# Performance work log

Measured on AMD Instinct MI355X. Metric: run time of the kernel, lower is better.

Reference implementation:

```python
import jax, jax.numpy as jnp
import numpy as np

HEADS = 16
D_MODEL = 1024
D_K = D_MODEL // HEADS
BATCH = 4
SEQ = 1024
NEG_BIG = -1000000000.0


def setup_inputs() -> dict:
    key = jax.random.key(0)
    ks = jax.random.split(key, 7)
    s = 1.0 / np.sqrt(D_MODEL)
    return {
        "q": jax.random.normal(ks[0], (BATCH, SEQ, D_MODEL), jnp.float32),
        "k": jax.random.normal(ks[1], (BATCH, SEQ, D_MODEL), jnp.float32),
        "v": jax.random.normal(ks[2], (BATCH, SEQ, D_MODEL), jnp.float32),
        "Wq": jax.random.normal(ks[3], (D_MODEL, D_MODEL), jnp.float32) * s,
        "Wk": jax.random.normal(ks[4], (D_MODEL, D_MODEL), jnp.float32) * s,
        "Wv": jax.random.normal(ks[5], (D_MODEL, D_MODEL), jnp.float32) * s,
        "Wo": jax.random.normal(ks[6], (D_MODEL, D_MODEL), jnp.float32) * s,
    }


def reference(q, k, v, Wq, Wk, Wv, Wo):
    bs = q.shape[0]
    residual = q
    # torch Linear(bias=False): x @ W.T ; then the module's quirky reshape
    # view(bs, h, -1, d_k) on the contiguous [bs, seq, d_model] buffer.
    qh = (q @ Wq.T).reshape(bs, HEADS, -1, D_K)   # [b, h, s, d_k]
    kh = (k @ Wk.T).reshape(bs, HEADS, -1, D_K)
    vh = (v @ Wv.T).reshape(bs, HEADS, -1, D_K)
    scores = jnp.einsum("bhqd,bhkd->bhqk", qh, kh) / jnp.sqrt(
        jnp.asarray(D_K, qh.dtype))
    # data-dependent mask: exact-zero scores get -1e9 before softmax
    scores = jnp.where(scores == 0, jnp.asarray(NEG_BIG, scores.dtype), scores)
    attn = jax.nn.softmax(scores, axis=-1)  # dropout is identity in eval mode
    out = jnp.einsum("bhqk,bhkd->bhqd", attn, vh)  # [b, h, s, d_k]
    concat = jnp.swapaxes(out, 1, 2).reshape(bs, -1, D_MODEL)
    return concat @ Wo.T + residual
```

## Files before the change

### kernel.cpp

```cpp
#include <hip/hip_runtime.h>
#include <stdint.h>

typedef __bf16 bf16x8 __attribute__((ext_vector_type(8)));
typedef __bf16 bf16x2v __attribute__((ext_vector_type(2)));
typedef float f32x4 __attribute__((ext_vector_type(4)));
typedef uint16_t u16x8 __attribute__((ext_vector_type(8)));
typedef uint32_t u32x2 __attribute__((ext_vector_type(2)));
typedef short s16x4 __attribute__((ext_vector_type(4)));

#define DMODEL 1024
#define K1SC 0.1803368801111244f

__device__ __forceinline__ uint16_t bfc(float f) {
  __bf16 h = (__bf16)f;
  return __builtin_bit_cast(uint16_t, h);
}
__device__ __forceinline__ uint32_t pk32(float a, float b) {
  bf16x2v t = {(__bf16)a, (__bf16)b};
  return __builtin_bit_cast(uint32_t, t);
}
__device__ __forceinline__ void gld16(const void* src, void* dst) {
  __builtin_amdgcn_global_load_lds((const __attribute__((address_space(1))) void*)src,
                                   (__attribute__((address_space(3))) void*)dst, 16, 0, 0);
}

__global__ __launch_bounds__(256, 2)
void gemm_qkv_kernel(const float* __restrict__ A0, const float* __restrict__ A1,
                     const float* __restrict__ A2, const float* __restrict__ W0,
                     const float* __restrict__ W1, const float* __restrict__ W2,
                     uint16_t* __restrict__ C0, uint16_t* __restrict__ C1,
                     uint16_t* __restrict__ C2) {
  int orig = blockIdx.x;
  int lin = (orig & 7) * 96 + (orig >> 3);
  int z = lin >> 8, rem = lin & 255;
  int m0 = (rem >> 3) * 128, n0 = (rem & 7) * 128;

  const float* A  = z == 0 ? A0 : (z == 1 ? A1 : A2);
  const float* Bw = z == 0 ? W0 : (z == 1 ? W1 : W2);
  uint16_t* C = z == 0 ? C0 : (z == 1 ? C1 : C2);
  const float osc = (z == 0) ? K1SC : 1.0f;

  __shared__ __align__(16) char As[2][128 * 64];
  __shared__ __align__(16) char Bs[2][128 * 64];
  const int t = threadIdx.x;
  const int lane = t & 63;
  const int w = t >> 6;
  const int wr = w >> 1, wc = w & 1;
  const int lr = lane & 15, ksl = lane >> 4;

  const int srow = t >> 2, sch = t & 3;
  const float* pa = A + (size_t)(m0 + srow) * DMODEL + sch * 8;
  const float* pb = Bw + (size_t)(n0 + srow) * DMODEL + sch * 8;
  const int sd = srow * 64 + ((sch ^ (srow & 3)) * 16);

  f32x4 la0, la1, la2, la3, lb0, lb1, lb2, lb3;
  auto LOAD = [&]() {
    la0 = *(const f32x4*)pa;           la1 = *(const f32x4*)(pa + 4);
    la2 = *(const f32x4*)(pa + 65536); la3 = *(const f32x4*)(pa + 65540);
    lb0 = *(const f32x4*)pb;           lb1 = *(const f32x4*)(pb + 4);
    lb2 = *(const f32x4*)(pb + 65536); lb3 = *(const f32x4*)(pb + 65540);
  };
  auto pack2 = [](f32x4 x, f32x4 y) {
    u16x8 r;
#pragma unroll
    for (int j = 0; j < 4; ++j) { r[j] = bfc(x[j]); r[4 + j] = bfc(y[j]); }
    return r;
  };
  auto STORE = [&](int buf) {
    char* ab = &As[buf][0];
    char* bb = &Bs[buf][0];
    *(u16x8*)(ab + sd) = pack2(la0, la1);
    *(u16x8*)(ab + sd + 4096) = pack2(la2, la3);
    *(u16x8*)(bb + sd) = pack2(lb0, lb1);
    *(u16x8*)(bb + sd + 4096) = pack2(lb2, lb3);
  };

  f32x4 acc[4][4];
#pragma unroll
  for (int m = 0; m < 4; ++m)
#pragma unroll
    for (int n = 0; n < 4; ++n) acc[m][n] = (f32x4){0.f, 0.f, 0.f, 0.f};

  LOAD();
  STORE(0);
  __syncthreads();

  const int co = (ksl ^ (lr & 3)) * 16;

  int cur = 0;
#pragma unroll 1
  for (int kt = 0; kt < 32; ++kt) {
    if (kt < 31) { pa += 32; pb += 32; LOAD(); }
    const char* Ab = &As[cur][0];
    const char* Bb = &Bs[cur][0];
    bf16x8 af[4], bfv[4];
#pragma unroll
    for (int m = 0; m < 4; ++m)
      af[m] = *(const bf16x8*)(Ab + (wr * 64 + m * 16 + lr) * 64 + co);
#pragma unroll
    for (int n = 0; n < 4; ++n)
      bfv[n] = *(const bf16x8*)(Bb + (wc * 64 + n * 16 + lr) * 64 + co);
    __builtin_amdgcn_s_setprio(1);
#pragma unroll
    for (int m = 0; m < 4; ++m)
#pragma unroll
      for (int n = 0; n < 4; ++n)
        acc[m][n] = __builtin_amdgcn_mfma_f32_16x16x32_bf16(af[m], bfv[n], acc[m][n], 0, 0, 0);
    __builtin_amdgcn_s_setprio(0);
    if (kt < 31) STORE(cur ^ 1);
    __syncthreads();
    cur ^= 1;
  }

#pragma unroll
  for (int m = 0; m < 4; ++m) {
#pragma unroll
    for (int n = 0; n < 4; ++n) {
      int col = n0 + wc * 64 + n * 16 + lr;
#pragma unroll
      for (int r = 0; r < 4; ++r) {
        int row = m0 + wr * 64 + m * 16 + ksl * 4 + r;
        C[(size_t)row * DMODEL + col] = bfc(acc[m][n][r] * osc);
      }
    }
  }
}

__global__ __launch_bounds__(256, 4)
void gemm_o_kernel(const uint16_t* __restrict__ Ac, const float* __restrict__ Bw,
                   float* __restrict__ Cf, const float* __restrict__ resid) {
  int orig = blockIdx.x;
  int lin = (orig & 7) * 64 + (orig >> 3);
  int m0 = (lin >> 3) * 64, n0 = (lin & 7) * 128;

  __shared__ __align__(16) char As[2][64 * 64];
  __shared__ __align__(16) char Bs[2][128 * 64];
  const int t = threadIdx.x;
  const int lane = t & 63;
  const int w = t >> 6;
  const int wr = w >> 1, wc = w & 1;
  const int lr = lane & 15, ksl = lane >> 4;

  const int srow = t >> 2, sch = t & 3;
  const uint16_t* pc = Ac + (size_t)(m0 + srow) * DMODEL + sch * 8;
  const float* pb = Bw + (size_t)(n0 + srow) * DMODEL + sch * 8;
  const int sd = srow * 64 + ((sch ^ (srow & 3)) * 16);

  u16x8 lc;
  f32x4 lb0, lb1, lb2, lb3;
  auto LOAD = [&]() {
    lc = *(const u16x8*)pc;
    lb0 = *(const f32x4*)pb;           lb1 = *(const f32x4*)(pb + 4);
    lb2 = *(const f32x4*)(pb + 65536); lb3 = *(const f32x4*)(pb + 65540);
  };
  auto pack2 = [](f32x4 x, f32x4 y) {
    u16x8 r;
#pragma unroll
    for (int j = 0; j < 4; ++j) { r[j] = bfc(x[j]); r[4 + j] = bfc(y[j]); }
    return r;
  };
  auto STORE = [&](int buf) {
    *(u16x8*)(&As[buf][0] + sd) = lc;
    char* bb = &Bs[buf][0];
    *(u16x8*)(bb + sd) = pack2(lb0, lb1);
    *(u16x8*)(bb + sd + 4096) = pack2(lb2, lb3);
  };

  f32x4 acc[2][4];
#pragma unroll
  for (int m = 0; m < 2; ++m)
#pragma unroll
    for (int n = 0; n < 4; ++n) acc[m][n] = (f32x4){0.f, 0.f, 0.f, 0.f};

  LOAD();
  STORE(0);
  __syncthreads();

  const int co = (ksl ^ (lr & 3)) * 16;

  int cur = 0;
#pragma unroll 1
  for (int kt = 0; kt < 32; ++kt) {
    if (kt < 31) { pc += 32; pb += 32; LOAD(); }
    const char* Ab = &As[cur][0];
    const char* Bb = &Bs[cur][0];
    bf16x8 af[2], bfv[4];
#pragma unroll
    for (int m = 0; m < 2; ++m)
      af[m] = *(const bf16x8*)(Ab + (wr * 32 + m * 16 + lr) * 64 + co);
#pragma unroll
    for (int n = 0; n < 4; ++n)
      bfv[n] = *(const bf16x8*)(Bb + (wc * 64 + n * 16 + lr) * 64 + co);
    __builtin_amdgcn_s_setprio(1);
#pragma unroll
    for (int m = 0; m < 2; ++m)
#pragma unroll
      for (int n = 0; n < 4; ++n)
        acc[m][n] = __builtin_amdgcn_mfma_f32_16x16x32_bf16(af[m], bfv[n], acc[m][n], 0, 0, 0);
    __builtin_amdgcn_s_setprio(0);
    if (kt < 31) STORE(cur ^ 1);
    __syncthreads();
    cur ^= 1;
  }

#pragma unroll
  for (int m = 0; m < 2; ++m) {
#pragma unroll
    for (int n = 0; n < 4; ++n) {
      int col = n0 + wc * 64 + n * 16 + lr;
#pragma unroll
      for (int r = 0; r < 4; ++r) {
        int row = m0 + wr * 32 + m * 16 + ksl * 4 + r;
        size_t idx = (size_t)row * DMODEL + col;
        Cf[idx] = acc[m][n][r] + resid[idx];
      }
    }
  }
}

__global__ __launch_bounds__(256, 4)
void attn_mfma_kernel(const uint16_t* __restrict__ Pq, const uint16_t* __restrict__ Pk,
                      const uint16_t* __restrict__ Pv, uint16_t* __restrict__ Cc) {
  __shared__ __align__(16) uint16_t Ks[2][64 * 64];
  __shared__ __align__(16) uint16_t Vts[2][64 * 64];

  const int t = threadIdx.x;
  const int w = t >> 6;
  const int lane = t & 63;
  const int lr = lane & 15;
  const int ksl = lane >> 4;
  int orig = blockIdx.x;
  int lin = (orig & 7) * 128 + (orig >> 3);
  const int bh = lin >> 4, qt = lin & 15;
  const int b = bh >> 4, h = bh & 15;

  const uint16_t* Qb = Pq + (size_t)bh * 65536 + (size_t)qt * 4096;
  const uint16_t* Kb = Pk + (size_t)bh * 65536;
  const uint16_t* Vb = Pv + (size_t)bh * 65536;

  bf16x8 qf0, qf1;
  {
    const uint16_t* qrow = Qb + (size_t)(w * 16 + lr) * 64 + ksl * 8;
    qf0 = *(const bf16x8*)(qrow);
    qf1 = *(const bf16x8*)(qrow + 32);
  }

  f32x4 Oa[4];
#pragma unroll
  for (int n = 0; n < 4; ++n) Oa[n] = (f32x4){0.f, 0.f, 0.f, 0.f};
  f32x4 lsum4 = {0.f, 0.f, 0.f, 0.f};

  const int sw = (lr & 7) << 4;
  const int p2 = t & 31;
  const int c8 = t >> 5;

  int qko[4][2], pvo[4][4], wvo[8];
#pragma unroll
  for (int n = 0; n < 4; ++n) {
#pragma unroll
    for (int c = 0; c < 2; ++c) qko[n][c] = (n * 16 + lr) * 128 + ((c * 64 + ksl * 16) ^ sw);
#pragma unroll
    for (int nd = 0; nd < 4; ++nd) pvo[n][nd] = (nd * 16 + lr) * 128 + ((n * 32 + ksl * 8) ^ sw);
  }
#pragma unroll
  for (int i = 0; i < 8; ++i) {
    int d = c8 * 8 + i;
    wvo[i] = d * 128 + ((p2 * 4) ^ ((d & 7) << 4));
  }

  const int sr0 = t >> 3;
  const int sc0 = (((t & 7) * 16) ^ ((sr0 & 7) << 4)) >> 1;
  const uint16_t* srcK = Kb + (size_t)sr0 * 64 + sc0;
  const uint16_t* srcV = Vb + (size_t)(p2 * 2) * 64 + c8 * 8;
  const int kd0 = t * 16, kd1 = (256 + t) * 16;

  char* kb0 = (char*)&Ks[0][0];
  char* kb1 = (char*)&Ks[1][0];
  char* vb0 = (char*)&Vts[0][0];
  char* vb1 = (char*)&Vts[1][0];

  u16x8 va, vb2;
  auto stageK = [&](char* kbuf) {
    gld16(srcK, kbuf + kd0);
    gld16(srcK + 2048, kbuf + kd1);
  };
  auto loadV = [&]() {
    va = *(const u16x8*)srcV;
    vb2 = *(const u16x8*)(srcV + 64);
  };
  auto writeV = [&](char* vbuf) {
#pragma unroll
    for (int i = 0; i < 8; ++i) {
      uint32_t val = (uint32_t)va[i] | ((uint32_t)vb2[i] << 16);
      *(uint32_t*)(vbuf + wvo[i]) = val;
    }
  };

  stageK(kb0);
  loadV();
  writeV(vb0);
  __syncthreads();

  const char* kcur = kb0; char* knx = kb1;
  const char* vcur = vb0; char* vnx = vb1;

#pragma unroll 1
  for (int kt = 0; kt < 16; ++kt) {
    if (kt < 15) { srcK += 4096; stageK(knx); srcV += 4096; loadV(); }

    f32x4 S[4];
#pragma unroll
    for (int n = 0; n < 4; ++n) S[n] = (f32x4){0.f, 0.f, 0.f, 0.f};
    __builtin_amdgcn_s_setprio(1);
#pragma unroll
    for (int n = 0; n < 4; ++n) {
      bf16x8 kf0 = *(const bf16x8*)(kcur + qko[n][0]);
      bf16x8 kf1 = *(const bf16x8*)(kcur + qko[n][1]);
      S[n] = __builtin_amdgcn_mfma_f32_16x16x32_bf16(kf0, qf0, S[n], 0, 0, 0);
      S[n] = __builtin_amdgcn_mfma_f32_16x16x32_bf16(kf1, qf1, S[n], 0, 0, 0);
    }
    __builtin_amdgcn_s_setprio(0);

    f32x4 psum = {0.f, 0.f, 0.f, 0.f};
    f32x4 p4[4];
#pragma unroll
    for (int n = 0; n < 4; ++n) {
#pragma unroll
      for (int r = 0; r < 4; ++r) {
        float x = S[n][r];
        float e = __builtin_amdgcn_exp2f(x);
        p4[n][r] = (x == 0.f) ? 0.f : e;
      }
      psum += p4[n];
    }
    lsum4 += psum;

    __builtin_amdgcn_s_setprio(1);
#pragma unroll
    for (int n = 0; n < 4; ++n) {
      u32x2 pa32 = {pk32(p4[n][0], p4[n][1]), pk32(p4[n][2], p4[n][3])};
      s16x4 pa = __builtin_bit_cast(s16x4, pa32);
#pragma unroll
      for (int nd = 0; nd < 4; ++nd) {
        s16x4 vf = *(const s16x4*)(vcur + pvo[n][nd]);
        Oa[nd] = __builtin_amdgcn_mfma_f32_16x16x16bf16_1k(pa, vf, Oa[nd], 0, 0, 0);
      }
    }
    __builtin_amdgcn_s_setprio(0);

    if (kt < 15) writeV(vnx);
    __syncthreads();
    const char* tk = kcur; kcur = knx; knx = (char*)tk;
    const char* tv = vcur; vcur = vnx; vnx = (char*)tv;
  }

  float lrow = (lsum4[0] + lsum4[1]) + (lsum4[2] + lsum4[3]);
  lrow += __shfl_xor(lrow, 16);
  lrow += __shfl_xor(lrow, 32);
  f32x4 inv4;
#pragma unroll
  for (int r = 0; r < 4; ++r) inv4[r] = 1.f / __shfl(lrow, ksl * 4 + r);

  uint16_t* dst = Cc + (size_t)b * 1048576 + (size_t)(qt * 64 + w * 16) * 1024 + h * 64;
#pragma unroll
  for (int r = 0; r < 4; ++r) {
    int qq = ksl * 4 + r;
#pragma unroll
    for (int n = 0; n < 4; ++n) {
      dst[qq * 1024 + n * 16 + lr] = bfc(Oa[n][r] * inv4[r]);
    }
  }
}

extern "C" void kernel_launch(void* const* d_in, const int* in_sizes, int n_in,
                              void* d_out, int out_size, void* d_ws, size_t ws_size,
                              hipStream_t stream) {
  const float* q  = (const float*)d_in[0];
  const float* k  = (const float*)d_in[1];
  const float* v  = (const float*)d_in[2];
  const float* Wq = (const float*)d_in[3];
  const float* Wk = (const float*)d_in[4];
  const float* Wv = (const float*)d_in[5];
  const float* Wo = (const float*)d_in[6];
  float* out = (float*)d_out;
  char* ws = (char*)d_ws;
  const size_t MB = 1u << 20;
  uint16_t* Pq = (uint16_t*)(ws + 0 * MB);
  uint16_t* Pk = (uint16_t*)(ws + 8 * MB);
  uint16_t* Pv = (uint16_t*)(ws + 16 * MB);
  uint16_t* Cc = (uint16_t*)(ws + 24 * MB);

  gemm_qkv_kernel<<<768, 256, 0, stream>>>(q, k, v, Wq, Wk, Wv, Pq, Pk, Pv);

  attn_mfma_kernel<<<1024, 256, 0, stream>>>(Pq, Pk, Pv, Cc);

  gemm_o_kernel<<<512, 256, 0, stream>>>(Cc, Wo, out, q);
}
```

Baseline: 100.8 us.

## Deepen projection GEMM global-load prefetch to two register stages

The projection GEMM now keeps two register sets of fp32 tiles, so global loads are issued two k-steps ahead of their LDS store rather than one. The main loop is unrolled by two and alternates the buffers. The aim is to hide more global memory latency behind the MFMA work. The cost is a doubled staging register footprint, which may reduce occupancy.

Result: slower. 103.0 us (+2.2%).

```diff
diff --git a/kernel.cpp b/kernel.cpp
--- a/kernel.cpp
+++ b/kernel.cpp
@@ -53,12 +53,21 @@
   const float* pb = Bw + (size_t)(n0 + srow) * DMODEL + sch * 8;
   const int sd = srow * 64 + ((sch ^ (srow & 3)) * 16);
 
-  f32x4 la0, la1, la2, la3, lb0, lb1, lb2, lb3;
-  auto LOAD = [&]() {
-    la0 = *(const f32x4*)pa;           la1 = *(const f32x4*)(pa + 4);
-    la2 = *(const f32x4*)(pa + 65536); la3 = *(const f32x4*)(pa + 65540);
-    lb0 = *(const f32x4*)pb;           lb1 = *(const f32x4*)(pb + 4);
-    lb2 = *(const f32x4*)(pb + 65536); lb3 = *(const f32x4*)(pb + 65540);
+  f32x4 a0[4], b0[4], a1[4], b1[4];
+
+  auto LOAD0 = [&]() {
+    a0[0] = *(const f32x4*)pa;           a0[1] = *(const f32x4*)(pa + 4);
+    a0[2] = *(const f32x4*)(pa + 65536); a0[3] = *(const f32x4*)(pa + 65540);
+    b0[0] = *(const f32x4*)pb;           b0[1] = *(const f32x4*)(pb + 4);
+    b0[2] = *(const f32x4*)(pb + 65536); b0[3] = *(const f32x4*)(pb + 65540);
+    pa += 32; pb += 32;
+  };
+  auto LOAD1 = [&]() {
+    a1[0] = *(const f32x4*)pa;           a1[1] = *(const f32x4*)(pa + 4);
+    a1[2] = *(const f32x4*)(pa + 65536); a1[3] = *(const f32x4*)(pa + 65540);
+    b1[0] = *(const f32x4*)pb;           b1[1] = *(const f32x4*)(pb + 4);
+    b1[2] = *(const f32x4*)(pb + 65536); b1[3] = *(const f32x4*)(pb + 65540);
+    pa += 32; pb += 32;
   };
   auto pack2 = [](f32x4 x, f32x4 y) {
     u16x8 r;
@@ -66,13 +75,21 @@
     for (int j = 0; j < 4; ++j) { r[j] = bfc(x[j]); r[4 + j] = bfc(y[j]); }
     return r;
   };
-  auto STORE = [&](int buf) {
+  auto STORE0 = [&](int buf) {
     char* ab = &As[buf][0];
     char* bb = &Bs[buf][0];
-    *(u16x8*)(ab + sd) = pack2(la0, la1);
-    *(u16x8*)(ab + sd + 4096) = pack2(la2, la3);
-    *(u16x8*)(bb + sd) = pack2(lb0, lb1);
-    *(u16x8*)(bb + sd + 4096) = pack2(lb2, lb3);
+    *(u16x8*)(ab + sd) = pack2(a0[0], a0[1]);
+    *(u16x8*)(ab + sd + 4096) = pack2(a0[2], a0[3]);
+    *(u16x8*)(bb + sd) = pack2(b0[0], b0[1]);
+    *(u16x8*)(bb + sd + 4096) = pack2(b0[2], b0[3]);
+  };
+  auto STORE1 = [&](int buf) {
+    char* ab = &As[buf][0];
+    char* bb = &Bs[buf][0];
+    *(u16x8*)(ab + sd) = pack2(a1[0], a1[1]);
+    *(u16x8*)(ab + sd + 4096) = pack2(a1[2], a1[3]);
+    *(u16x8*)(bb + sd) = pack2(b1[0], b1[1]);
+    *(u16x8*)(bb + sd + 4096) = pack2(b1[2], b1[3]);
   };
 
   f32x4 acc[4][4];
@@ -81,16 +98,15 @@
 #pragma unroll
     for (int n = 0; n < 4; ++n) acc[m][n] = (f32x4){0.f, 0.f, 0.f, 0.f};
 
-  LOAD();
-  STORE(0);
+  LOAD0();
+  STORE0(0);
+  LOAD0();
+  LOAD1();
   __syncthreads();
 
   const int co = (ksl ^ (lr & 3)) * 16;
 
-  int cur = 0;
-#pragma unroll 1
-  for (int kt = 0; kt < 32; ++kt) {
-    if (kt < 31) { pa += 32; pb += 32; LOAD(); }
+  auto MFMA = [&](int cur) {
     const char* Ab = &As[cur][0];
     const char* Bb = &Bs[cur][0];
     bf16x8 af[4], bfv[4];
@@ -107,7 +123,19 @@
       for (int n = 0; n < 4; ++n)
         acc[m][n] = __builtin_amdgcn_mfma_f32_16x16x32_bf16(af[m], bfv[n], acc[m][n], 0, 0, 0);
     __builtin_amdgcn_s_setprio(0);
-    if (kt < 31) STORE(cur ^ 1);
+  };
+
+  int cur = 0;
+#pragma unroll 1
+  for (int kt2 = 0; kt2 < 32; kt2 += 2) {
+    MFMA(cur);
+    if (kt2 < 31) STORE0(cur ^ 1);
+    if (kt2 + 3 <= 31) LOAD0();
+    __syncthreads();
+    cur ^= 1;
+    MFMA(cur);
+    if (kt2 + 2 <= 31) STORE1(cur ^ 1);
+    if (kt2 + 4 <= 31) LOAD1();
     __syncthreads();
     cur ^= 1;
   }
```
